# Kernel tuning notes

Hardware: AMD Instinct MI355X
Metric: run time of the kernel (lower is better)

## Reference

```python
import jax, jax.numpy as jnp
import numpy as np

B, L, H, D_IN = 64, 4096, 128, 3

def setup_inputs() -> dict:
    key = jax.random.key(0)
    ks = jax.random.split(key, 9)
    def lin_w(k, fan_in, shape):
        bound = 1.0 / np.sqrt(fan_in)
        return jax.random.uniform(k, shape, jnp.float32, -bound, bound)
    return {
        "x": jax.random.normal(ks[0], (B, L, D_IN), jnp.float32),
        "Wp": lin_w(ks[1], D_IN, (D_IN, H)), "bp": lin_w(ks[2], D_IN, (H,)),
        "Wz": lin_w(ks[3], H, (H, H)),      "bz": lin_w(ks[4], H, (H,)),
        "Wh": lin_w(ks[5], H, (H, H)),      "bh": lin_w(ks[6], H, (H,)),
        "Wg": lin_w(ks[7], H, (H, 1)),      "bg": lin_w(ks[8], H, (1,)),
    }

def reference(x, Wp, bp, Wz, bz, Wh, bh, Wg, bg):
    # Batched projections across all timesteps (B, L, H)
    inp = x @ Wp + bp                      # input_proj
    z = jax.nn.sigmoid(inp @ Wz + bz)      # update gate
    h_tilde = jnp.tanh(inp @ Wh + bh)      # candidate
    # Linear recurrence h_t = a_t * h_{t-1} + b_t, h_{-1} = 0
    a = 1.0 - z
    b = z * h_tilde
    def combine(c1, c2):
        a1, b1 = c1
        a2, b2 = c2
        return (a1 * a2, b1 * a2 + b2)
    _, h = jax.lax.associative_scan(combine, (a, b), axis=1)  # h_t (since h_{-1}=0)
    # Readout uses h BEFORE the update at each step: preds_t = gauss_head(h_{t-1})
    h_prev = jnp.concatenate([jnp.zeros_like(h[:, :1]), h[:, :-1]], axis=1)
    preds = h_prev @ Wg + bg               # (B, L, 1)
    return preds
```

## Files before the change

kernel.cpp:

```cpp
#include <hip/hip_runtime.h>
#include <hip/hip_bf16.h>
#include <stdint.h>

#define B_   64
#define L_   4096
#define H_   128
#define HG_  16
#define NG_  8
#define TI_  128
#define NIT_ 32
#define PADI 136

#define ABI(t,h) ((t)*17 + ((h) ^ (((t)>>2) & 15)))

typedef __attribute__((ext_vector_type(8))) short short8;
typedef __attribute__((ext_vector_type(4))) float floatx4;

#define LOG2E 1.44269504088896340736f

__device__ __forceinline__ unsigned short f2bf(float f){
    unsigned int u = __float_as_uint(f);
    u += 0x7FFFu + ((u >> 16) & 1u);
    return (unsigned short)(u >> 16);
}
__device__ __forceinline__ unsigned int pack2(float lo, float hi){
    __hip_bfloat162 h = __float22bfloat162_rn(make_float2(lo, hi));
    return *reinterpret_cast<unsigned int*>(&h);
}

__global__ __launch_bounds__(512, 4)
void fused_rnn(const float* __restrict__ x,
               const float* __restrict__ Wp, const float* __restrict__ bp,
               const float* __restrict__ Wz, const float* __restrict__ bz,
               const float* __restrict__ Wh, const float* __restrict__ bh,
               const float* __restrict__ Wg,
               float* __restrict__ partials)
{
    __shared__ __align__(16) unsigned short s_inp[TI_*PADI];
    __shared__ unsigned int s_ab[TI_*17];
    __shared__ float s_y[TI_*17];

    const int bid = blockIdx.x;
    const int bb  = bid >> 3;
    const int g   = bid & 7;
    const int tid = threadIdx.x;
    const int wv = tid >> 6, lane = tid & 63, quad = lane >> 4, l15 = lane & 15;

    const int tg  = tid >> 5;
    const int cg  = tid & 31;
    const int rh  = tid >> 5;
    const int rs  = tid & 31;
    const int dt  = tid >> 2;
    const int dp  = tid & 3;

    {
        unsigned short* s_w = s_inp;
        const int gate = tid >> 8;
        const int r    = tid & 255;
        const int n    = r >> 4;
        const int k0   = (r & 15) * 8;
        const float* Wsrc = gate ? Wh : Wz;
        #pragma unroll
        for (int j = 0; j < 8; ++j){
            int k = k0 + j;
            s_w[gate*2048 + n*H_ + k] = f2bf(Wsrc[(size_t)k*H_ + g*HG_ + n]);
        }
    }
    __syncthreads();

    short8 bfr[2][4];
    #pragma unroll
    for (int G = 0; G < 2; ++G)
        #pragma unroll
        for (int kk = 0; kk < 4; ++kk)
            bfr[G][kk] = *(const short8*)&s_inp[G*2048 + l15*H_ + kk*32 + quad*8];
    const float biasz = bz[g*HG_ + l15];
    const float biash = bh[g*HG_ + l15];
    const float wgv   = Wg[g*HG_ + rh];
    float w0[4], w1[4], w2[4], bc[4];
    #pragma unroll
    for (int m = 0; m < 4; ++m){
        w0[m] = Wp[cg*4+m]; w1[m] = Wp[H_+cg*4+m]; w2[m] = Wp[2*H_+cg*4+m];
        bc[m] = bp[cg*4+m];
    }
    float h_run = 0.0f;
    __syncthreads();

    float* pbase = partials + (size_t)(g*B_ + bb)*L_;

    for (int it = 0; it < NIT_; ++it){
        {
            #pragma unroll
            for (int j = 0; j < 8; ++j){
                int t = tg*8 + j;
                const float* xr = x + ((size_t)bb*L_ + it*TI_ + t)*3;
                float x0 = xr[0], x1 = xr[1], x2 = xr[2];
                float v0 = fmaf(x2, w2[0], fmaf(x1, w1[0], fmaf(x0, w0[0], bc[0])));
                float v1 = fmaf(x2, w2[1], fmaf(x1, w1[1], fmaf(x0, w0[1], bc[1])));
                float v2 = fmaf(x2, w2[2], fmaf(x1, w1[2], fmaf(x0, w0[2], bc[2])));
                float v3 = fmaf(x2, w2[3], fmaf(x1, w1[3], fmaf(x0, w0[3], bc[3])));
                uint2 st; st.x = pack2(v0, v1); st.y = pack2(v2, v3);
                *(uint2*)&s_inp[t*PADI + cg*4] = st;
            }
        }
        __syncthreads();

        {
            floatx4 accz = (floatx4){0.f,0.f,0.f,0.f};
            floatx4 acch = (floatx4){0.f,0.f,0.f,0.f};
            #pragma unroll
            for (int kk = 0; kk < 4; ++kk){
                short8 af = *(const short8*)&s_inp[(wv*16 + l15)*PADI + kk*32 + quad*8];
                accz = __builtin_amdgcn_mfma_f32_16x16x32_bf16(af, bfr[0][kk], accz, 0, 0, 0);
                acch = __builtin_amdgcn_mfma_f32_16x16x32_bf16(af, bfr[1][kk], acch, 0, 0, 0);
            }
            #pragma unroll
            for (int e = 0; e < 4; ++e){
                int t = wv*16 + quad*4 + e;
                float vz = accz[e] + biasz;
                float a  = __builtin_amdgcn_rcpf(1.0f + __builtin_amdgcn_exp2f(vz * LOG2E));
                float vh = acch[e] + biash;
                float ex = __builtin_amdgcn_exp2f(2.0f*LOG2E*vh);
                float th = 1.0f - 2.0f*__builtin_amdgcn_rcpf(ex + 1.0f);
                s_ab[ABI(t, l15)] = pack2(a, th);
            }
        }
        __syncthreads();

        {
            float aj[4], bj[4];
            float P = 1.0f, Q = 0.0f;
            #pragma unroll
            for (int j = 0; j < 4; ++j){
                int t = rs*4 + j;
                unsigned int u = s_ab[ABI(t, rh)];
                float a  = __uint_as_float(u << 16);
                float th = __uint_as_float(u & 0xffff0000u);
                float b  = fmaf(-a, th, th);
                aj[j] = a; bj[j] = b;
                Q = fmaf(a, Q, b);
                P *= a;
            }
            #pragma unroll
            for (int d = 1; d < 32; d <<= 1){
                float pP = __shfl_up(P, d, 32);
                float pH = __shfl_up(Q, d, 32);
                if (rs >= d){
                    Q = fmaf(P, pH, Q);
                    P = P * pP;
                }
            }
            float eP = __shfl_up(P, 1, 32);
            float eH = __shfl_up(Q, 1, 32);
            if (rs == 0){ eP = 1.0f; eH = 0.0f; }
            float tP = __shfl(P, 31, 32);
            float tH = __shfl(Q, 31, 32);
            float hh = fmaf(eP, h_run, eH);
            h_run = fmaf(tP, h_run, tH);
            #pragma unroll
            for (int j = 0; j < 4; ++j){
                int t = rs*4 + j;
                s_y[ABI(t, rh)] = wgv * hh;
                hh = fmaf(aj[j], hh, bj[j]);
            }
        }
        __syncthreads();

        {
            float s = s_y[ABI(dt, dp*4+0)] + s_y[ABI(dt, dp*4+1)]
                    + s_y[ABI(dt, dp*4+2)] + s_y[ABI(dt, dp*4+3)];
            s += __shfl_xor(s, 1, 64);
            s += __shfl_xor(s, 2, 64);
            if (dp == 0)
                pbase[it*TI_ + dt] = s;
        }
    }
}

__global__ __launch_bounds__(1024)
void gather(const floatx4* __restrict__ partials, const float* __restrict__ bg,
            floatx4* __restrict__ preds)
{
    size_t i = (size_t)blockIdx.x*1024 + threadIdx.x;
    const size_t S = (size_t)B_ * L_ / 4;
    float b = bg[0];
    floatx4 v = partials[i];
    #pragma unroll
    for (int gg = 1; gg < NG_; ++gg) v += partials[gg*S + i];
    v[0] += b; v[1] += b; v[2] += b; v[3] += b;
    preds[i] = v;
}

extern "C" void kernel_launch(void* const* d_in, const int* in_sizes, int n_in,
                              void* d_out, int out_size, void* d_ws, size_t ws_size,
                              hipStream_t stream){
    const float* x  = (const float*)d_in[0];
    const float* Wp = (const float*)d_in[1];
    const float* bp = (const float*)d_in[2];
    const float* Wz = (const float*)d_in[3];
    const float* bz = (const float*)d_in[4];
    const float* Wh = (const float*)d_in[5];
    const float* bh = (const float*)d_in[6];
    const float* Wg = (const float*)d_in[7];
    const float* bg = (const float*)d_in[8];
    float* preds = (float*)d_out;

    uint8_t* w8 = (uint8_t*)d_ws;
    float* partials = (float*)w8;

    hipLaunchKernelGGL(fused_rnn, dim3(B_*NG_), dim3(512), 0, stream,
                       x, Wp, bp, Wz, bz, Wh, bh, Wg, partials);
    hipLaunchKernelGGL(gather, dim3(B_*L_/4096), dim3(1024), 0, stream,
                       (const floatx4*)partials, bg, (floatx4*)preds);
}
```

Before: 162.8 us.

## Split input projection into separate kernel and prefetch bf16 tiles in RNN loop

Moves the x@Wp+bp projection out of the recurrent kernel into its own kernel that writes a bf16 (B,L,H) buffer to workspace. The fused kernel then loads each 128-step tile from that buffer with register prefetch of the next tile, overlapped with the scan. Blocks double to 1024 threads, with each wave doing one gate's MFMA and the scan running over 64 lanes with 2 steps per lane. LDS reads use XOR swizzling instead of padding. This trades an extra 64 MB global write and read for removing the per-channel projection work that every gate-group block repeated.

Result: slower. 219.5 us (+34.8%).

```diff
diff --git a/kernel.cpp b/kernel.cpp
--- a/kernel.cpp
+++ b/kernel.cpp
@@ -9,168 +9,179 @@
 #define NG_  8
 #define TI_  128
 #define NIT_ 32
-#define PADI 136
+#define LOG2E 1.44269504088896340736f
 
 #define ABI(t,h) ((t)*17 + ((h) ^ (((t)>>2) & 15)))
 
 typedef __attribute__((ext_vector_type(8))) short short8;
 typedef __attribute__((ext_vector_type(4))) float floatx4;
-
-#define LOG2E 1.44269504088896340736f
 
 __device__ __forceinline__ unsigned short f2bf(float f){
     unsigned int u = __float_as_uint(f);
     u += 0x7FFFu + ((u >> 16) & 1u);
     return (unsigned short)(u >> 16);
 }
-__device__ __forceinline__ unsigned int pack2(float lo, float hi){
-    __hip_bfloat162 h = __float22bfloat162_rn(make_float2(lo, hi));
-    return *reinterpret_cast<unsigned int*>(&h);
-}
-
-__global__ __launch_bounds__(512, 4)
-void fused_rnn(const float* __restrict__ x,
-               const float* __restrict__ Wp, const float* __restrict__ bp,
+
+__global__ __launch_bounds__(1024)
+void inp_proj(const float* __restrict__ x, const float* __restrict__ Wp,
+              const float* __restrict__ bp, unsigned short* __restrict__ inp_g)
+{
+    const int tid = threadIdx.x;
+    const int h0 = (tid & 15) * 8;
+    const size_t id = (size_t)blockIdx.x*1024 + tid;
+    const size_t t = id >> 4;
+    const float* xr = x + t*3;
+    const float x0 = xr[0], x1 = xr[1], x2 = xr[2];
+    floatx4 wa0 = *(const floatx4*)&Wp[h0],      wb0 = *(const floatx4*)&Wp[h0+4];
+    floatx4 wa1 = *(const floatx4*)&Wp[H_+h0],   wb1 = *(const floatx4*)&Wp[H_+h0+4];
+    floatx4 wa2 = *(const floatx4*)&Wp[2*H_+h0], wb2 = *(const floatx4*)&Wp[2*H_+h0+4];
+    floatx4 ba  = *(const floatx4*)&bp[h0],      bb4 = *(const floatx4*)&bp[h0+4];
+    short8 pk;
+    #pragma unroll
+    for (int m = 0; m < 4; ++m){
+        float v = fmaf(x2, wa2[m], fmaf(x1, wa1[m], fmaf(x0, wa0[m], ba[m])));
+        pk[m] = (short)f2bf(v);
+        float w = fmaf(x2, wb2[m], fmaf(x1, wb1[m], fmaf(x0, wb0[m], bb4[m])));
+        pk[4+m] = (short)f2bf(w);
+    }
+    *(short8*)&inp_g[t*H_ + h0] = pk;
+}
+
+__global__ __launch_bounds__(1024, 4)
+void fused_rnn(const unsigned short* __restrict__ inp_g,
                const float* __restrict__ Wz, const float* __restrict__ bz,
                const float* __restrict__ Wh, const float* __restrict__ bh,
                const float* __restrict__ Wg,
                float* __restrict__ partials)
 {
-    __shared__ __align__(16) unsigned short s_inp[TI_*PADI];
+    __shared__ __align__(16) unsigned short s_inp[TI_*H_];
     __shared__ unsigned int s_ab[TI_*17];
     __shared__ float s_y[TI_*17];
 
     const int bid = blockIdx.x;
-    const int bb  = bid >> 3;
-    const int g   = bid & 7;
+    const int bb  = bid & 63;
+    const int g   = bid >> 6;
     const int tid = threadIdx.x;
     const int wv = tid >> 6, lane = tid & 63, quad = lane >> 4, l15 = lane & 15;
-
-    const int tg  = tid >> 5;
-    const int cg  = tid & 31;
-    const int rh  = tid >> 5;
-    const int rs  = tid & 31;
-    const int dt  = tid >> 2;
-    const int dp  = tid & 3;
+    const int G = wv >> 3, tile = wv & 7;
 
     {
-        unsigned short* s_w = s_inp;
-        const int gate = tid >> 8;
-        const int r    = tid & 255;
-        const int n    = r >> 4;
-        const int k0   = (r & 15) * 8;
-        const float* Wsrc = gate ? Wh : Wz;
+        const float* Wsrc = (tid >= 512) ? Wh : Wz;
+        const int r  = tid & 511;
+        const int n  = r >> 5;
+        const int k0 = (r & 31) * 4;
+        unsigned short* dst = s_inp + (tid >> 9)*2048 + n*H_ + k0;
+        const float* src = Wsrc + (size_t)k0*H_ + g*HG_ + n;
         #pragma unroll
-        for (int j = 0; j < 8; ++j){
-            int k = k0 + j;
-            s_w[gate*2048 + n*H_ + k] = f2bf(Wsrc[(size_t)k*H_ + g*HG_ + n]);
-        }
+        for (int j = 0; j < 4; ++j)
+            dst[j] = f2bf(src[(size_t)j*H_]);
     }
     __syncthreads();
 
-    short8 bfr[2][4];
+    short8 bfr[4];
     #pragma unroll
-    for (int G = 0; G < 2; ++G)
-        #pragma unroll
-        for (int kk = 0; kk < 4; ++kk)
-            bfr[G][kk] = *(const short8*)&s_inp[G*2048 + l15*H_ + kk*32 + quad*8];
-    const float biasz = bz[g*HG_ + l15];
-    const float biash = bh[g*HG_ + l15];
-    const float wgv   = Wg[g*HG_ + rh];
-    float w0[4], w1[4], w2[4], bc[4];
-    #pragma unroll
-    for (int m = 0; m < 4; ++m){
-        w0[m] = Wp[cg*4+m]; w1[m] = Wp[H_+cg*4+m]; w2[m] = Wp[2*H_+cg*4+m];
-        bc[m] = bp[cg*4+m];
-    }
+    for (int kk = 0; kk < 4; ++kk)
+        bfr[kk] = *(const short8*)&s_inp[G*2048 + l15*H_ + kk*32 + quad*8];
+    const float biasv = (G ? bh : bz)[g*HG_ + l15];
+    const float wgv   = Wg[g*HG_ + wv];
+
+    const int t0 = tid >> 4, cl = tid & 15;
+    const char* gsrc = (const char*)(inp_g + (size_t)bb*L_*H_)
+                     + (size_t)t0*256 + (size_t)((cl ^ (t0 & 15)) << 4);
+    char* ldst = (char*)s_inp + tid*16;
+
+    floatx4 ld0 = *(const floatx4*)gsrc;
+    floatx4 ld1 = *(const floatx4*)(gsrc + 16384);
+    __syncthreads();
+    *(floatx4*)ldst           = ld0;
+    *(floatx4*)(ldst + 16384) = ld1;
+    __syncthreads();
+
     float h_run = 0.0f;
-    __syncthreads();
-
-    float* pbase = partials + (size_t)(g*B_ + bb)*L_;
-
+    float* pbase = partials + ((size_t)(g*B_ + bb))*L_;
+
+    const char* abase = (const char*)s_inp + (tile*16 + l15)*256
+                      + ((quad ^ (l15 & 3)) << 4);
+    const int kx = (l15 >> 2) & 3;
+
+    #pragma unroll 1
     for (int it = 0; it < NIT_; ++it){
         {
-            #pragma unroll
-            for (int j = 0; j < 8; ++j){
-                int t = tg*8 + j;
-                const float* xr = x + ((size_t)bb*L_ + it*TI_ + t)*3;
-                float x0 = xr[0], x1 = xr[1], x2 = xr[2];
-                float v0 = fmaf(x2, w2[0], fmaf(x1, w1[0], fmaf(x0, w0[0], bc[0])));
-                float v1 = fmaf(x2, w2[1], fmaf(x1, w1[1], fmaf(x0, w0[1], bc[1])));
-                float v2 = fmaf(x2, w2[2], fmaf(x1, w1[2], fmaf(x0, w0[2], bc[2])));
-                float v3 = fmaf(x2, w2[3], fmaf(x1, w1[3], fmaf(x0, w0[3], bc[3])));
-                uint2 st; st.x = pack2(v0, v1); st.y = pack2(v2, v3);
-                *(uint2*)&s_inp[t*PADI + cg*4] = st;
-            }
-        }
-        __syncthreads();
-
-        {
-            floatx4 accz = (floatx4){0.f,0.f,0.f,0.f};
-            floatx4 acch = (floatx4){0.f,0.f,0.f,0.f};
+            floatx4 acc = (floatx4){0.f,0.f,0.f,0.f};
             #pragma unroll
             for (int kk = 0; kk < 4; ++kk){
-                short8 af = *(const short8*)&s_inp[(wv*16 + l15)*PADI + kk*32 + quad*8];
-                accz = __builtin_amdgcn_mfma_f32_16x16x32_bf16(af, bfr[0][kk], accz, 0, 0, 0);
-                acch = __builtin_amdgcn_mfma_f32_16x16x32_bf16(af, bfr[1][kk], acch, 0, 0, 0);
+                short8 af = *(const short8*)(abase + ((kk ^ kx) << 6));
+                acc = __builtin_amdgcn_mfma_f32_16x16x32_bf16(af, bfr[kk], acc, 0, 0, 0);
             }
             #pragma unroll
             for (int e = 0; e < 4; ++e){
-                int t = wv*16 + quad*4 + e;
-                float vz = accz[e] + biasz;
-                float a  = __builtin_amdgcn_rcpf(1.0f + __builtin_amdgcn_exp2f(vz * LOG2E));
-                float vh = acch[e] + biash;
-                float ex = __builtin_amdgcn_exp2f(2.0f*LOG2E*vh);
-                float th = 1.0f - 2.0f*__builtin_amdgcn_rcpf(ex + 1.0f);
-                s_ab[ABI(t, l15)] = pack2(a, th);
+                int t = tile*16 + quad*4 + e;
+                float v = acc[e] + biasv;
+                float r;
+                if (G == 0){
+                    r = __builtin_amdgcn_rcpf(1.0f + __builtin_amdgcn_exp2f(v * LOG2E));
+                } else {
+                    float ex = __builtin_amdgcn_exp2f(2.0f*LOG2E*v);
+                    r = 1.0f - 2.0f*__builtin_amdgcn_rcpf(ex + 1.0f);
+                }
+                ((unsigned short*)s_ab)[ABI(t, l15)*2 + G] = f2bf(r);
             }
         }
         __syncthreads();
 
+        floatx4 nld0, nld1;
+        const bool more = (it + 1 < NIT_);
+        if (more){
+            const char* gs = gsrc + (size_t)(it+1)*32768;
+            nld0 = *(const floatx4*)gs;
+            nld1 = *(const floatx4*)(gs + 16384);
+        }
+
         {
-            float aj[4], bj[4];
-            float P = 1.0f, Q = 0.0f;
+            int t = lane*2;
+            unsigned int u0 = s_ab[ABI(t,   wv)];
+            unsigned int u1 = s_ab[ABI(t+1, wv)];
+            float a0  = __uint_as_float(u0 << 16);
+            float th0 = __uint_as_float(u0 & 0xffff0000u);
+            float b0  = fmaf(-a0, th0, th0);
+            float a1  = __uint_as_float(u1 << 16);
+            float th1 = __uint_as_float(u1 & 0xffff0000u);
+            float b1  = fmaf(-a1, th1, th1);
+            float P = a0 * a1;
+            float Q = fmaf(a1, b0, b1);
             #pragma unroll
-            for (int j = 0; j < 4; ++j){
-                int t = rs*4 + j;
-                unsigned int u = s_ab[ABI(t, rh)];
-                float a  = __uint_as_float(u << 16);
-                float th = __uint_as_float(u & 0xffff0000u);
-                float b  = fmaf(-a, th, th);
-                aj[j] = a; bj[j] = b;
-                Q = fmaf(a, Q, b);
-                P *= a;
-            }
-            #pragma unroll
-            for (int d = 1; d < 32; d <<= 1){
-                float pP = __shfl_up(P, d, 32);
-                float pH = __shfl_up(Q, d, 32);
-                if (rs >= d){
-                    Q = fmaf(P, pH, Q);
+            for (int d = 1; d < 64; d <<= 1){
+                float pP = __shfl_up(P, d, 64);
+                float pQ = __shfl_up(Q, d, 64);
+                if (lane >= d){
+                    Q = fmaf(P, pQ, Q);
                     P = P * pP;
                 }
             }
-            float eP = __shfl_up(P, 1, 32);
-            float eH = __shfl_up(Q, 1, 32);
-            if (rs == 0){ eP = 1.0f; eH = 0.0f; }
-            float tP = __shfl(P, 31, 32);
-            float tH = __shfl(Q, 31, 32);
-            float hh = fmaf(eP, h_run, eH);
-            h_run = fmaf(tP, h_run, tH);
-            #pragma unroll
-            for (int j = 0; j < 4; ++j){
-                int t = rs*4 + j;
-                s_y[ABI(t, rh)] = wgv * hh;
-                hh = fmaf(aj[j], hh, bj[j]);
-            }
+            float eP = __shfl_up(P, 1, 64);
+            float eQ = __shfl_up(Q, 1, 64);
+            if (lane == 0){ eP = 1.0f; eQ = 0.0f; }
+            float tP = __shfl(P, 63, 64);
+            float tQ = __shfl(Q, 63, 64);
+            float hh = fmaf(eP, h_run, eQ);
+            h_run = fmaf(tP, h_run, tQ);
+            s_y[ABI(t, wv)] = wgv * hh;
+            hh = fmaf(a0, hh, b0);
+            s_y[ABI(t+1, wv)] = wgv * hh;
+        }
+
+        if (more){
+            *(floatx4*)ldst           = nld0;
+            *(floatx4*)(ldst + 16384) = nld1;
         }
         __syncthreads();
 
         {
-            float s = s_y[ABI(dt, dp*4+0)] + s_y[ABI(dt, dp*4+1)]
-                    + s_y[ABI(dt, dp*4+2)] + s_y[ABI(dt, dp*4+3)];
+            int dt = tid >> 3, dp = tid & 7;
+            float s = s_y[ABI(dt, dp*2)] + s_y[ABI(dt, dp*2 + 1)];
             s += __shfl_xor(s, 1, 64);
             s += __shfl_xor(s, 2, 64);
+            s += __shfl_xor(s, 4, 64);
             if (dp == 0)
                 pbase[it*TI_ + dt] = s;
         }
@@ -206,10 +217,12 @@
     float* preds = (float*)d_out;
 
     uint8_t* w8 = (uint8_t*)d_ws;
-    float* partials = (float*)w8;
-
-    hipLaunchKernelGGL(fused_rnn, dim3(B_*NG_), dim3(512), 0, stream,
-                       x, Wp, bp, Wz, bz, Wh, bh, Wg, partials);
+    unsigned short* inp_g = (unsigned short*)w8;
+    float* partials = (float*)(w8 + 67108864);
+
+    hipLaunchKernelGGL(inp_proj, dim3(4096), dim3(1024), 0, stream, x, Wp, bp, inp_g);
+    hipLaunchKernelGGL(fused_rnn, dim3(B_*NG_), dim3(1024), 0, stream,
+                       inp_g, Wz, bz, Wh, bh, Wg, partials);
     hipLaunchKernelGGL(gather, dim3(B_*L_/4096), dim3(1024), 0, stream,
                        (const floatx4*)partials, bg, (floatx4*)preds);
 }
```
